# Kernel optimization log

Hardware: AMD Instinct MI355X
Metric: run time of the kernel (lower is better)

## Reference

```python
import jax, jax.numpy as jnp
import numpy as np

B, N, H, E = 16, 256, 128, 16
LN_EPS = 1e-5


def setup_inputs() -> dict:
    key = jax.random.key(0)
    ks = jax.random.split(key, 16)
    def lin(k, fan_in, fan_out):
        bound = 1.0 / np.sqrt(fan_in)
        kw, kb = jax.random.split(k)
        W = jax.random.uniform(kw, (fan_in, fan_out), jnp.float32, -bound, bound)
        b = jax.random.uniform(kb, (fan_out,), jnp.float32, -bound, bound)
        return W, b
    dW1, db1 = lin(ks[0], 1, E)
    dW2, db2 = lin(ks[1], E, E)
    uW1, ub1 = lin(ks[2], 2 * H + E, 2 * E)
    uW2, ub2 = lin(ks[3], 2 * E, E)
    nW1, nb1 = lin(ks[4], E, H // 2)
    nW2, nb2 = lin(ks[5], H // 2, H)
    return {
        "node_embeddings": jax.random.normal(ks[6], (B, N, H), jnp.float32),
        "distance_matrix": jax.random.uniform(ks[7], (B, N, N), jnp.float32),
        "visited": jax.random.randint(ks[8], (B, N), 0, 2) > 0,
        "dW1": dW1, "db1": db1, "dW2": dW2, "db2": db2,
        "uW1": uW1, "ub1": ub1,
        "ln_g": jnp.ones((2 * E,), jnp.float32), "ln_b": jnp.zeros((2 * E,), jnp.float32),
        "uW2": uW2, "ub2": ub2,
        "nW1": nW1, "nb1": nb1, "nW2": nW2, "nb2": nb2,
    }


def _layernorm(x, g, b):
    mu = jnp.mean(x, axis=-1, keepdims=True)
    var = jnp.mean((x - mu) ** 2, axis=-1, keepdims=True)
    return (x - mu) * jax.lax.rsqrt(var + LN_EPS) * g + b


def reference(node_embeddings, distance_matrix, visited,
              dW1, db1, dW2, db2,
              uW1, ub1, ln_g, ln_b, uW2, ub2,
              nW1, nb1, nW2, nb2):
    Bn, Nn, Hn = node_embeddings.shape
    # distance encoder: [B,N,N,1] -> [B,N,N,E]
    d = distance_matrix[..., None]
    dist_feat = jax.nn.relu(d @ dW1 + db1) @ dW2 + db2
    # pairwise concat [node_i, node_j, dist] -> edge MLP
    node_i = jnp.broadcast_to(node_embeddings[:, :, None, :], (Bn, Nn, Nn, Hn))
    node_j = jnp.broadcast_to(node_embeddings[:, None, :, :], (Bn, Nn, Nn, Hn))
    edge_input = jnp.concatenate([node_i, node_j, dist_feat], axis=-1)  # [B,N,N,2H+E]
    h = _layernorm(edge_input @ uW1 + ub1, ln_g, ln_b)
    edge_features = jax.nn.relu(h) @ uW2 + ub2  # [B,N,N,E]
    # mask by visited rows (scale by 0.5 where visited)
    scale = 1.0 - visited.astype(edge_features.dtype) * 0.5  # [B,N]
    edge_features = edge_features * scale[:, :, None, None]
    # mean over j, then node MLP
    pooled = jnp.mean(edge_features, axis=2)  # [B,N,E]
    edge_messages = jax.nn.relu(pooled @ nW1 + nb1) @ nW2 + nb2  # [B,N,H]
    return edge_features, edge_messages
```

## Files before the change

kernel.cpp:

```cpp
#include <hip/hip_runtime.h>

#define NB 16
#define NN 256
#define NH 128
#define NE 16

typedef float v4f  __attribute__((ext_vector_type(4)));
typedef short bf16x8 __attribute__((ext_vector_type(8)));
typedef unsigned int uint;

constexpr long long EF_ELEMS = (long long)NB * NN * NN * NE;


__global__ __launch_bounds__(256) void k_prep_proj(
    const float* __restrict__ node, const float* __restrict__ uW1,
    const float* __restrict__ dW1, const float* __restrict__ db1,
    const float* __restrict__ dW2, const float* __restrict__ db2,
    const float* __restrict__ ub1,
    float* __restrict__ bps, float* __restrict__ albe,
    float* __restrict__ Pi, float* __restrict__ Pj)
{
    const int t = threadIdx.x;
    if (blockIdx.x == 1024) {
        __shared__ float sM[512];
        __shared__ float sBp[16];
        __shared__ float sA[16], sB[16];
        for (int i = t; i < 512; i += 256) {
            const int k = i >> 5, c = i & 31;
            float s = 0.f;
#pragma unroll
            for (int e = 0; e < 16; ++e)
                s = fmaf(dW2[k * 16 + e], uW1[(256 + e) * 32 + c], s);
            sM[i] = s;
        }
        if (t < 16) { sA[t] = dW1[t]; sB[t] = db1[t]; }
        __syncthreads();
        if (t < 16) {
            const float a = sA[t];
            const float x = (a != 0.f) ? (-sB[t] / a) : -1e30f;
            int r = 0;
            for (int q = 0; q < 16; ++q) {
                const float aq = sA[q];
                const float xq = (aq != 0.f) ? (-sB[q] / aq) : -1e30f;
                r += (xq < x) || (xq == x && q < t);
            }
            sBp[r] = x;
        }
        __syncthreads();
        if (t < 16) bps[t] = sBp[t];
        for (int i = t; i < 544; i += 256) {
            const int s = i >> 5, c = i & 31;
            float dt;
            if (s == 0)       dt = sBp[0] - 1.0f;
            else if (s == 16) dt = sBp[15] + 1.0f;
            else              dt = 0.5f * (sBp[s - 1] + sBp[s]);
            float alpha = 0.f, beta = 0.f;
#pragma unroll
            for (int k = 0; k < 16; ++k) {
                if (fmaf(sA[k], dt, sB[k]) > 0.f) {
                    const float m = sM[k * 32 + c];
                    alpha = fmaf(sA[k], m, alpha);
                    beta  = fmaf(sB[k], m, beta);
                }
            }
            float c2 = ub1[c];
#pragma unroll
            for (int e = 0; e < 16; ++e)
                c2 = fmaf(db2[e], uW1[(256 + e) * 32 + c], c2);
            albe[s * 68 + c]      = alpha;
            albe[s * 68 + 32 + c] = beta + c2;
        }
        for (int i = 1156 + t; i < 1280; i += 256) albe[i] = 0.f;
    } else {
        const int r = t >> 6, sub = t & 63;
        const int row = blockIdx.x * 4 + r;
        __shared__ float nrow[4][128];
        nrow[r][sub]      = node[(size_t)row * 128 + sub];
        nrow[r][sub + 64] = node[(size_t)row * 128 + 64 + sub];
        __syncthreads();
        const int c = sub & 31;
        const int half = sub >> 5;
        const float* w = uW1 + half * 128 * 32 + c;
        float s = 0.f;
#pragma unroll 8
        for (int k = 0; k < 128; ++k)
            s = fmaf(nrow[r][k], w[k * 32], s);
        (half ? Pj : Pi)[(size_t)row * 32 + c] = s;
    }
}

__global__ __launch_bounds__(256, 4) void k_edge6(
    const float* __restrict__ dist, const int* __restrict__ visited,
    const float* __restrict__ ln_g, const float* __restrict__ ln_b,
    const float* __restrict__ uW2, const float* __restrict__ ub2,
    const float* __restrict__ bps, const float* __restrict__ albe_g,
    const float* __restrict__ Pi, const float* __restrict__ Pj,
    const float* __restrict__ nW1, const float* __restrict__ nb1,
    const float* __restrict__ nW2, const float* __restrict__ nb2,
    float* __restrict__ ef_out, float* __restrict__ msg_out)
{
    const int row0 = blockIdx.x * 4;
    const int b = row0 >> 8;
    const int j = threadIdx.x;

    __shared__ float albe_s[1280];
    __shared__ uint  h_lds[256 * 17];
    __shared__ float red2[4][4][16];
    __shared__ float pool_s[4][16];
    __shared__ float hid_s[4][64];

    {
        const float4* ag = reinterpret_cast<const float4*>(albe_g);
        float4* as = reinterpret_cast<float4*>(albe_s);
        for (int q = j; q < 320; q += 256) as[q] = ag[q];
    }

    const int lane = j & 63, wv = j >> 6;
    const int eRow = lane & 15;
    const int g    = lane >> 4;

    bf16x8 ahi, alo;
    {
        union { uint u[4]; bf16x8 v; } Uhi, Ulo;
#pragma unroll
        for (int p = 0; p < 4; ++p) {
            const int q = g * 4 + p;
            const float w0 = uW2[(2 * q) * 16 + eRow];
            const float w1 = uW2[(2 * q + 1) * 16 + eRow];
            uint W00, W11, Whi, Wlo;
            asm("v_cvt_pk_bf16_f32 %0, %1, %2" : "=v"(W00) : "v"(w0), "v"(w0));
            asm("v_cvt_pk_bf16_f32 %0, %1, %2" : "=v"(W11) : "v"(w1), "v"(w1));
            const float w0h = __uint_as_float(W00 << 16);
            const float w1h = __uint_as_float(W11 << 16);
            asm("v_cvt_pk_bf16_f32 %0, %1, %2" : "=v"(Whi) : "v"(w0), "v"(w1));
            asm("v_cvt_pk_bf16_f32 %0, %1, %2" : "=v"(Wlo) : "v"(w0 - w0h), "v"(w1 - w1h));
            Uhi.u[p] = Whi;
            Ulo.u[p] = Wlo;
        }
        ahi = Uhi.v;
        alo = Ulo.v;
    }

    float dq[4];
#pragma unroll
    for (int r = 0; r < 4; ++r)
        dq[r] = dist[(size_t)(row0 + r) * NN + j];

    const float4 ub2v = *reinterpret_cast<const float4*>(&ub2[g * 4]);
    const float4* pj4 = reinterpret_cast<const float4*>(Pj + ((size_t)(b * NN + j)) * 32);
    float4 pj[8];
#pragma unroll
    for (int q = 0; q < 8; ++q) pj[q] = pj4[q];

    __syncthreads();

    uint hw[16];
    auto compute_h = [&](int r) {
        const float d = dq[r];
        int seg = 0;
#pragma unroll
        for (int k = 0; k < 16; ++k) seg += (d > bps[k]) ? 1 : 0;
        const float* ab = &albe_s[seg * 68];
        const float* PiRow = Pi + (size_t)(row0 + r) * 32;
        float pre[32];
#pragma unroll
        for (int q = 0; q < 8; ++q) {
            const float4 al = *reinterpret_cast<const float4*>(&ab[q * 4]);
            const float4 be = *reinterpret_cast<const float4*>(&ab[32 + q * 4]);
            pre[q * 4 + 0] = PiRow[q * 4 + 0] + pj[q].x + fmaf(d, al.x, be.x);
            pre[q * 4 + 1] = PiRow[q * 4 + 1] + pj[q].y + fmaf(d, al.y, be.y);
            pre[q * 4 + 2] = PiRow[q * 4 + 2] + pj[q].z + fmaf(d, al.z, be.z);
            pre[q * 4 + 3] = PiRow[q * 4 + 3] + pj[q].w + fmaf(d, al.w, be.w);
        }
        float s0 = 0.f, s1 = 0.f, s2 = 0.f, s3 = 0.f;
#pragma unroll
        for (int c = 0; c < 32; c += 4) { s0 += pre[c]; s1 += pre[c+1]; s2 += pre[c+2]; s3 += pre[c+3]; }
        const float mu = ((s0 + s1) + (s2 + s3)) * (1.f / 32.f);
        float v0 = 0.f, v1 = 0.f, v2 = 0.f, v3 = 0.f;
#pragma unroll
        for (int c = 0; c < 32; c += 4) {
            pre[c]   -= mu; v0 = fmaf(pre[c],   pre[c],   v0);
            pre[c+1] -= mu; v1 = fmaf(pre[c+1], pre[c+1], v1);
            pre[c+2] -= mu; v2 = fmaf(pre[c+2], pre[c+2], v2);
            pre[c+3] -= mu; v3 = fmaf(pre[c+3], pre[c+3], v3);
        }
        const float rstd = rsqrtf(fmaf((v0 + v1) + (v2 + v3), 1.f / 32.f, 1e-5f));
#pragma unroll
        for (int c = 0; c < 32; ++c)
            pre[c] = fmaxf(fmaf(pre[c] * rstd, ln_g[c], ln_b[c]), 0.f);
#pragma unroll
        for (int q = 0; q < 16; ++q) {
            uint rr;
            asm("v_cvt_pk_bf16_f32 %0, %1, %2" : "=v"(rr) : "v"(pre[2*q]), "v"(pre[2*q+1]));
            hw[q] = rr;
        }
    };
    auto write_h = [&]() {
        uint* hrow = &h_lds[j * 17];
        *reinterpret_cast<uint4*>(hrow + 0)  = make_uint4(hw[0],  hw[1],  hw[2],  hw[3]);
        *reinterpret_cast<uint4*>(hrow + 4)  = make_uint4(hw[4],  hw[5],  hw[6],  hw[7]);
        *reinterpret_cast<uint4*>(hrow + 8)  = make_uint4(hw[8],  hw[9],  hw[10], hw[11]);
        *reinterpret_cast<uint4*>(hrow + 12) = make_uint4(hw[12], hw[13], hw[14], hw[15]);
    };
    auto mfma_row = [&](int r) {
        const int row = row0 + r;
        const float scale = visited[row] ? 0.5f : 1.0f;
        v4f accsum = {0.f, 0.f, 0.f, 0.f};
#pragma unroll
        for (int t = 0; t < 4; ++t) {
            const int edge = wv * 64 + t * 16 + eRow;
            const bf16x8 bfr = *reinterpret_cast<const bf16x8*>(&h_lds[edge * 17 + g * 4]);
            v4f acc = {ub2v.x, ub2v.y, ub2v.z, ub2v.w};
            acc = __builtin_amdgcn_mfma_f32_16x16x32_bf16(alo, bfr, acc, 0, 0, 0);
            acc = __builtin_amdgcn_mfma_f32_16x16x32_bf16(ahi, bfr, acc, 0, 0, 0);
            acc[0] *= scale; acc[1] *= scale; acc[2] *= scale; acc[3] *= scale;
            *reinterpret_cast<v4f*>(ef_out + ((size_t)row * NN + edge) * 16 + g * 4) = acc;
            accsum += acc;
        }
#pragma unroll
        for (int rr = 0; rr < 4; ++rr) {
            float v = accsum[rr];
            v += __shfl_xor(v, 1);
            v += __shfl_xor(v, 2);
            v += __shfl_xor(v, 4);
            v += __shfl_xor(v, 8);
            accsum[rr] = v;
        }
        if (eRow == 0)
            *reinterpret_cast<v4f*>(&red2[r][wv][g * 4]) = accsum;
    };

    compute_h(0);
    write_h();
#pragma unroll
    for (int r = 0; r < 3; ++r) {
        compute_h(r + 1);
        mfma_row(r);
        write_h();
    }
    mfma_row(3);

    __syncthreads();

    if (j < 64) {
        const int r = j >> 4, e = j & 15;
        pool_s[r][e] = (red2[r][0][e] + red2[r][1][e] + red2[r][2][e] + red2[r][3][e])
                       * (1.f / 256.f);
    }
    __syncthreads();

    {
        const int r = j >> 6, u = j & 63;
        float s = nb1[u];
#pragma unroll
        for (int e = 0; e < 16; ++e)
            s = fmaf(pool_s[r][e], nW1[e * 64 + u], s);
        hid_s[r][u] = fmaxf(s, 0.f);
    }
    __syncthreads();

#pragma unroll
    for (int p = 0; p < 2; ++p) {
        const int idx = p * 256 + j;
        const int r = idx >> 7, o = idx & 127;
        float s = nb2[o];
#pragma unroll 8
        for (int q = 0; q < 64; ++q)
            s = fmaf(hid_s[r][q], nW2[q * 128 + o], s);
        msg_out[(size_t)(row0 + r) * 128 + o] = s;
    }
}

extern "C" void kernel_launch(void* const* d_in, const int* in_sizes, int n_in,
                              void* d_out, int out_size, void* d_ws, size_t ws_size,
                              hipStream_t stream)
{
    const float* node    = (const float*)d_in[0];
    const float* dist    = (const float*)d_in[1];
    const int*   visited = (const int*)  d_in[2];
    const float* dW1     = (const float*)d_in[3];
    const float* db1     = (const float*)d_in[4];
    const float* dW2     = (const float*)d_in[5];
    const float* db2     = (const float*)d_in[6];
    const float* uW1     = (const float*)d_in[7];
    const float* ub1     = (const float*)d_in[8];
    const float* ln_g    = (const float*)d_in[9];
    const float* ln_b    = (const float*)d_in[10];
    const float* uW2     = (const float*)d_in[11];
    const float* ub2     = (const float*)d_in[12];
    const float* nW1     = (const float*)d_in[13];
    const float* nb1     = (const float*)d_in[14];
    const float* nW2     = (const float*)d_in[15];
    const float* nb2     = (const float*)d_in[16];

    float* ws   = (float*)d_ws;
    float* bps  = ws;
    float* albe = ws + 16;
    float* Pi   = ws + 16 + 1280;
    float* Pj   = Pi + 4096 * 32;

    float* out = (float*)d_out;
    float* msg = out + EF_ELEMS;

    hipLaunchKernelGGL(k_prep_proj, dim3(1025), dim3(256), 0, stream,
                       node, uW1, dW1, db1, dW2, db2, ub1, bps, albe, Pi, Pj);
    hipLaunchKernelGGL(k_edge6, dim3(1024), dim3(256), 0, stream,
                       dist, visited, ln_g, ln_b, uW2, ub2, bps, albe, Pi, Pj,
                       nW1, nb1, nW2, nb2, out, msg);
}
```

Baseline: 41.53 us.

## Split prep projection K-loop, stage Pi in LDS, drop software pipelining in edge kernel

The prep kernel now runs 2 rows per block across 2049 blocks and splits each 128-long dot product into two 64-long halves combined with a cross-lane shuffle, which shortens the serial FMA chain. The edge kernel caches the Pi rows and visited scales in shared memory and registers at the start, pads the h tile stride from 17 to 20 words, and drops the 4-wide launch bound. The explicit compute/MFMA interleave across rows is replaced by a plain per-row loop. Without a barrier between the LDS write and the MFMA read, correctness relies on each wave reading only its own edges. Removing the overlap may lose latency hiding.

```diff
diff --git a/kernel.cpp b/kernel.cpp
--- a/kernel.cpp
+++ b/kernel.cpp
@@ -12,7 +12,7 @@
 constexpr long long EF_ELEMS = (long long)NB * NN * NN * NE;
 
 
-__global__ __launch_bounds__(256) void k_prep_proj(
+__global__ __launch_bounds__(256) void k_prep_proj2(
     const float* __restrict__ node, const float* __restrict__ uW1,
     const float* __restrict__ dW1, const float* __restrict__ db1,
     const float* __restrict__ dW2, const float* __restrict__ db2,
@@ -21,7 +21,7 @@
     float* __restrict__ Pi, float* __restrict__ Pj)
 {
     const int t = threadIdx.x;
-    if (blockIdx.x == 1024) {
+    if (blockIdx.x == 2048) {
         __shared__ float sM[512];
         __shared__ float sBp[16];
         __shared__ float sA[16], sB[16];
@@ -72,24 +72,27 @@
         }
         for (int i = 1156 + t; i < 1280; i += 256) albe[i] = 0.f;
     } else {
-        const int r = t >> 6, sub = t & 63;
-        const int row = blockIdx.x * 4 + r;
-        __shared__ float nrow[4][128];
-        nrow[r][sub]      = node[(size_t)row * 128 + sub];
-        nrow[r][sub + 64] = node[(size_t)row * 128 + 64 + sub];
+        const int r    = t >> 7;
+        const int half = (t >> 6) & 1;
+        const int ks   = (t >> 5) & 1;
+        const int c    = t & 31;
+        const int row  = blockIdx.x * 2 + r;
+        __shared__ float nrow[2][128];
+        nrow[r][t & 127] = node[(size_t)row * 128 + (t & 127)];
         __syncthreads();
-        const int c = sub & 31;
-        const int half = sub >> 5;
         const float* w = uW1 + half * 128 * 32 + c;
+        const int k0 = ks * 64;
         float s = 0.f;
 #pragma unroll 8
-        for (int k = 0; k < 128; ++k)
-            s = fmaf(nrow[r][k], w[k * 32], s);
-        (half ? Pj : Pi)[(size_t)row * 32 + c] = s;
+        for (int k = 0; k < 64; ++k)
+            s = fmaf(nrow[r][k0 + k], w[(size_t)(k0 + k) * 32], s);
+        s += __shfl_xor(s, 32);
+        if (!(t & 32))
+            (half ? Pj : Pi)[(size_t)row * 32 + c] = s;
     }
 }
 
-__global__ __launch_bounds__(256, 4) void k_edge6(
+__global__ __launch_bounds__(256) void k_edge7(
     const float* __restrict__ dist, const int* __restrict__ visited,
     const float* __restrict__ ln_g, const float* __restrict__ ln_b,
     const float* __restrict__ uW2, const float* __restrict__ ub2,
@@ -104,7 +107,8 @@
     const int j = threadIdx.x;
 
     __shared__ float albe_s[1280];
-    __shared__ uint  h_lds[256 * 17];
+    __shared__ uint  h_lds[256 * 20];
+    __shared__ float Pi_s[4][32];
     __shared__ float red2[4][4][16];
     __shared__ float pool_s[4][16];
     __shared__ float hid_s[4][64];
@@ -114,6 +118,11 @@
         float4* as = reinterpret_cast<float4*>(albe_s);
         for (int q = j; q < 320; q += 256) as[q] = ag[q];
     }
+    if (j < 128) Pi_s[j >> 5][j & 31] = Pi[(size_t)row0 * 32 + j];
+
+    float scv[4];
+#pragma unroll
+    for (int r = 0; r < 4; ++r) scv[r] = visited[row0 + r] ? 0.5f : 1.0f;
 
     const int lane = j & 63, wv = j >> 6;
     const int eRow = lane & 15;
@@ -154,24 +163,28 @@
 
     __syncthreads();
 
-    uint hw[16];
-    auto compute_h = [&](int r) {
+#pragma unroll
+    for (int r = 0; r < 4; ++r) {
+        const int row = row0 + r;
         const float d = dq[r];
+
         int seg = 0;
 #pragma unroll
         for (int k = 0; k < 16; ++k) seg += (d > bps[k]) ? 1 : 0;
         const float* ab = &albe_s[seg * 68];
-        const float* PiRow = Pi + (size_t)(row0 + r) * 32;
+
         float pre[32];
 #pragma unroll
         for (int q = 0; q < 8; ++q) {
+            const v4f piv = *reinterpret_cast<const v4f*>(&Pi_s[r][q * 4]);
             const float4 al = *reinterpret_cast<const float4*>(&ab[q * 4]);
             const float4 be = *reinterpret_cast<const float4*>(&ab[32 + q * 4]);
-            pre[q * 4 + 0] = PiRow[q * 4 + 0] + pj[q].x + fmaf(d, al.x, be.x);
-            pre[q * 4 + 1] = PiRow[q * 4 + 1] + pj[q].y + fmaf(d, al.y, be.y);
-            pre[q * 4 + 2] = PiRow[q * 4 + 2] + pj[q].z + fmaf(d, al.z, be.z);
-            pre[q * 4 + 3] = PiRow[q * 4 + 3] + pj[q].w + fmaf(d, al.w, be.w);
-        }
+            pre[q * 4 + 0] = piv.x + pj[q].x + fmaf(d, al.x, be.x);
+            pre[q * 4 + 1] = piv.y + pj[q].y + fmaf(d, al.y, be.y);
+            pre[q * 4 + 2] = piv.z + pj[q].z + fmaf(d, al.z, be.z);
+            pre[q * 4 + 3] = piv.w + pj[q].w + fmaf(d, al.w, be.w);
+        }
+
         float s0 = 0.f, s1 = 0.f, s2 = 0.f, s3 = 0.f;
 #pragma unroll
         for (int c = 0; c < 32; c += 4) { s0 += pre[c]; s1 += pre[c+1]; s2 += pre[c+2]; s3 += pre[c+3]; }
@@ -185,31 +198,31 @@
             pre[c+3] -= mu; v3 = fmaf(pre[c+3], pre[c+3], v3);
         }
         const float rstd = rsqrtf(fmaf((v0 + v1) + (v2 + v3), 1.f / 32.f, 1e-5f));
+
 #pragma unroll
         for (int c = 0; c < 32; ++c)
             pre[c] = fmaxf(fmaf(pre[c] * rstd, ln_g[c], ln_b[c]), 0.f);
-#pragma unroll
-        for (int q = 0; q < 16; ++q) {
-            uint rr;
-            asm("v_cvt_pk_bf16_f32 %0, %1, %2" : "=v"(rr) : "v"(pre[2*q]), "v"(pre[2*q+1]));
-            hw[q] = rr;
-        }
-    };
-    auto write_h = [&]() {
-        uint* hrow = &h_lds[j * 17];
-        *reinterpret_cast<uint4*>(hrow + 0)  = make_uint4(hw[0],  hw[1],  hw[2],  hw[3]);
-        *reinterpret_cast<uint4*>(hrow + 4)  = make_uint4(hw[4],  hw[5],  hw[6],  hw[7]);
-        *reinterpret_cast<uint4*>(hrow + 8)  = make_uint4(hw[8],  hw[9],  hw[10], hw[11]);
-        *reinterpret_cast<uint4*>(hrow + 12) = make_uint4(hw[12], hw[13], hw[14], hw[15]);
-    };
-    auto mfma_row = [&](int r) {
-        const int row = row0 + r;
-        const float scale = visited[row] ? 0.5f : 1.0f;
+        {
+            uint hw[16];
+#pragma unroll
+            for (int q = 0; q < 16; ++q) {
+                uint rr;
+                asm("v_cvt_pk_bf16_f32 %0, %1, %2" : "=v"(rr) : "v"(pre[2*q]), "v"(pre[2*q+1]));
+                hw[q] = rr;
+            }
+            uint* hrow = &h_lds[j * 20];
+            *reinterpret_cast<uint4*>(hrow + 0)  = make_uint4(hw[0],  hw[1],  hw[2],  hw[3]);
+            *reinterpret_cast<uint4*>(hrow + 4)  = make_uint4(hw[4],  hw[5],  hw[6],  hw[7]);
+            *reinterpret_cast<uint4*>(hrow + 8)  = make_uint4(hw[8],  hw[9],  hw[10], hw[11]);
+            *reinterpret_cast<uint4*>(hrow + 12) = make_uint4(hw[12], hw[13], hw[14], hw[15]);
+        }
+
+        const float scale = scv[r];
         v4f accsum = {0.f, 0.f, 0.f, 0.f};
 #pragma unroll
         for (int t = 0; t < 4; ++t) {
             const int edge = wv * 64 + t * 16 + eRow;
-            const bf16x8 bfr = *reinterpret_cast<const bf16x8*>(&h_lds[edge * 17 + g * 4]);
+            const bf16x8 bfr = *reinterpret_cast<const bf16x8*>(&h_lds[edge * 20 + g * 4]);
             v4f acc = {ub2v.x, ub2v.y, ub2v.z, ub2v.w};
             acc = __builtin_amdgcn_mfma_f32_16x16x32_bf16(alo, bfr, acc, 0, 0, 0);
             acc = __builtin_amdgcn_mfma_f32_16x16x32_bf16(ahi, bfr, acc, 0, 0, 0);
@@ -228,17 +241,7 @@
         }
         if (eRow == 0)
             *reinterpret_cast<v4f*>(&red2[r][wv][g * 4]) = accsum;
-    };
-
-    compute_h(0);
-    write_h();
-#pragma unroll
-    for (int r = 0; r < 3; ++r) {
-        compute_h(r + 1);
-        mfma_row(r);
-        write_h();
-    }
-    mfma_row(3);
+    }
 
     __syncthreads();
 
@@ -302,9 +305,9 @@
     float* out = (float*)d_out;
     float* msg = out + EF_ELEMS;
 
-    hipLaunchKernelGGL(k_prep_proj, dim3(1025), dim3(256), 0, stream,
+    hipLaunchKernelGGL(k_prep_proj2, dim3(2049), dim3(256), 0, stream,
                        node, uW1, dW1, db1, dW2, db2, ub1, bps, albe, Pi, Pj);
-    hipLaunchKernelGGL(k_edge6, dim3(1024), dim3(256), 0, stream,
+    hipLaunchKernelGGL(k_edge7, dim3(1024), dim3(256), 0, stream,
                        dist, visited, ln_g, ln_b, uW2, ub2, bps, albe, Pi, Pj,
                        nW1, nb1, nW2, nb2, out, msg);
 }
```

New measurement: 42.93 us. 3.4% more time.
